# Kernel tuning notes

Measured on AMD Instinct MI355X. Metric: run time of the kernel, lower is better.

The kernel has to match this reference:

```python
import jax, jax.numpy as jnp
import numpy as np

BETA = 0.25  # commitment_beta


def setup_inputs() -> dict:
    key = jax.random.key(0)
    k1, k2 = jax.random.split(key)
    x = jax.random.normal(k1, (16, 256, 32, 32), dtype=jnp.float32)
    # codebook weight: (n_embed + 1, embed_dim); last row is the padding idx (zeros)
    weight = jax.random.normal(k2, (8193, 256), dtype=jnp.float32) * 0.05
    weight = weight.at[-1].set(0.0)
    return {"x": x, "weight": weight}


def reference(x, weight):
    # Eval-mode forward of VectorQuantize2 (accept_image_fmap=True, no EMA update).
    B, C, H, W = x.shape
    xf = jnp.transpose(x, (0, 2, 3, 1)).reshape(B, H * W, C)  # b (h w) c
    emb = weight[:-1]  # [N, C], drop padding row
    # squared euclidean distance; argmin identical to torch.cdist argmin
    d2 = (
        jnp.sum(xf * xf, axis=-1, keepdims=True)
        - 2.0 * jnp.einsum("bnc,kc->bnk", xf, emb)
        + jnp.sum(emb * emb, axis=-1)
    )  # [B, HW, N]
    code = jnp.argmin(d2, axis=-1)  # [B, HW]
    x_q = emb[code]  # [B, HW, C]
    loss = BETA * jnp.mean((jax.lax.stop_gradient(x_q) - xf) ** 2) + jnp.mean(
        (x_q - jax.lax.stop_gradient(xf)) ** 2
    )
    # straight-through estimator
    xq_st = xf + jax.lax.stop_gradient(x_q - xf)
    xq_out = jnp.transpose(xq_st.reshape(B, H, W, C), (0, 3, 1, 2))  # b c h w
    code_out = code.reshape(B, H, W)
    return xq_out, loss, code_out
```

## Files before the change

### kernel.cpp

```cpp
#include <hip/hip_runtime.h>
#include <hip/hip_bf16.h>


#define N_ROWS   16384
#define KCODES   8192
#define DIM      256
#define LOSS_OFF 4194304
#define CODE_OFF 4194305
#define MARGIN_ACC 0.006f

typedef _Float16 half8  __attribute__((ext_vector_type(8)));
typedef _Float16 half4v __attribute__((ext_vector_type(4)));
typedef float    float4v __attribute__((ext_vector_type(4)));
typedef unsigned long long u64;

__device__ __forceinline__ unsigned umax32(unsigned a, unsigned b) { return a > b ? a : b; }
__device__ __forceinline__ unsigned umin32(unsigned a, unsigned b) { return a < b ? a : b; }
__device__ __forceinline__ void gll16(const _Float16* g, _Float16* l) {
  __builtin_amdgcn_global_load_lds((const __attribute__((address_space(1))) void*)g,
                                   (__attribute__((address_space(3))) void*)l, 16, 0, 0);
}


__global__ __launch_bounds__(256) void k_prep(const float* __restrict__ x, _Float16* __restrict__ xh,
                                              const float* __restrict__ wt, _Float16* __restrict__ eh,
                                              float* __restrict__ en2c, float* __restrict__ sxxp,
                                              double* __restrict__ dacc, unsigned* __restrict__ cnt) {
  __shared__ float lsx[128 * 65];
  __shared__ __align__(16) _Float16 ls[8192];
  __shared__ float es[32];
  int t = threadIdx.x;
  int lane = t & 63, wv = t >> 6;
  int bid = blockIdx.x;
  if (bid < 512) {
    if (bid == 0 && t == 0) { dacc[0] = 0.0; *cnt = 0u; }
    int blk = bid >> 2, cc = bid & 3;
    int row0 = blk * 128;
    int b    = row0 >> 10;
    int n0   = row0 & 1023;
    const float* xb = x + (size_t)b * 262144 + n0;
    int n_l = t & 127, cg = t >> 7;
    float sxx = 0.f;
    for (int j = 0; j < 32; ++j) {
      int c = cc * 64 + cg * 32 + j;
      float v = xb[(size_t)c * 1024 + n_l];
      sxx = fmaf(v, v, sxx);
      lsx[n_l * 65 + (c & 63)] = v;
    }
    __syncthreads();
#pragma unroll
    for (int i = 0; i < 4; ++i) {
      int unit = i * 256 + t;
      int rl = unit >> 3, p = unit & 7;
      const float* src = &lsx[rl * 65 + p * 8];
      half8 h;
#pragma unroll
      for (int k2 = 0; k2 < 8; ++k2) h[k2] = (_Float16)src[k2];
      int p7 = p ^ (rl & 7);
      *(half8*)&xh[(size_t)blk * 32768 + (size_t)cc * 8192 + (size_t)rl * 64 + p7 * 8] = h;
    }
#pragma unroll
    for (int d = 32; d; d >>= 1) sxx += __shfl_xor(sxx, d);
    __syncthreads();
    if (lane == 0) lsx[wv] = sxx;
    __syncthreads();
    if (t == 0) sxxp[bid] = lsx[0] + lsx[1] + lsx[2] + lsx[3];
  } else {
    int blk  = bid - 512;
    int k0 = blk * 32;
    const float* wb = wt + (size_t)k0 * 256;
    for (int i = 0; i < 8; ++i) {
      int lin = i * 1024 + t * 4;
      float4v v = *(const float4v*)&wb[lin];
      half4v h; float ss = 0.f;
#pragma unroll
      for (int j = 0; j < 4; ++j) { h[j] = (_Float16)v[j]; ss = fmaf(v[j], v[j], ss); }
      *(half4v*)&ls[lin] = h;
#pragma unroll
      for (int d = 32; d; d >>= 1) ss += __shfl_xor(ss, d);
      if (lane == 0) es[i * 4 + wv] = ss;
    }
    __syncthreads();
    size_t tb = (size_t)(k0 >> 7) * 32768;
    for (int i = 0; i < 4; ++i) {
      int u = i * 256 + t;
      int code_l = u >> 5;
      int cu = u & 31, chunk = cu >> 3, p = cu & 7;
      int kgl = k0 + code_l;
      int kg = p ^ (kgl & 7);
      half8 h = *(half8*)&ls[code_l * 256 + chunk * 64 + kg * 8];
      *(half8*)&eh[tb + (size_t)chunk * 8192 + (size_t)(kgl & 127) * 64 + p * 8] = h;
    }
    if (t < 32) en2c[k0 + t] = 32.0f - 0.5f * es[t];
  }
}

__global__ __launch_bounds__(256) void k_gemm(const _Float16* __restrict__ xh, const _Float16* __restrict__ eh,
                                              const float* __restrict__ en2c,
                                              u64* __restrict__ top2) {
  __shared__ __align__(16) _Float16 As[8192];
  __shared__ __align__(16) _Float16 Bs[8192];
  int t    = threadIdx.x;
  int bx   = blockIdx.x;
  int by   = blockIdx.y;
  int lane = t & 63, w = t >> 6;
  int wr = w & 1, wc = w >> 1;
  int ln15 = lane & 15, q = lane >> 4;
  int q4 = q * 4;

  const _Float16* Ag = eh + (size_t)bx * 32768;
  const _Float16* Bg = xh + (size_t)by * 32768;

  int kwave = bx * 128 + wr * 64;
  float4v cin[4];
#pragma unroll
  for (int mi = 0; mi < 4; ++mi) cin[mi] = *(const float4v*)&en2c[kwave + mi * 16 + q4];

  float4v acc[4][4];
#pragma unroll
  for (int mi = 0; mi < 4; ++mi)
#pragma unroll
    for (int ni = 0; ni < 4; ++ni) acc[mi][ni] = cin[mi];

  int so = (w * 64 + lane) * 8;
  int lo = w * 512;

  for (int ch = 0; ch < 4; ++ch) {
    if (ch) __syncthreads();
    const _Float16* ac = Ag + ch * 8192;
    const _Float16* bc = Bg + ch * 8192;
#pragma unroll
    for (int i = 0; i < 4; ++i) {
      gll16(ac + i * 2048 + so, As + i * 2048 + lo);
      gll16(bc + i * 2048 + so, Bs + i * 2048 + lo);
    }
    __syncthreads();
#pragma unroll
    for (int ks = 0; ks < 2; ++ks) {
      half8 af[4], bf[4];
#pragma unroll
      for (int mi = 0; mi < 4; ++mi) {
        int row = wr * 64 + mi * 16 + ln15;
        af[mi] = *(const half8*)&As[(row * 8 + ((ks * 4 + q) ^ (row & 7))) * 8];
      }
#pragma unroll
      for (int ni = 0; ni < 4; ++ni) {
        int row = wc * 64 + ni * 16 + ln15;
        bf[ni] = *(const half8*)&Bs[(row * 8 + ((ks * 4 + q) ^ (row & 7))) * 8];
      }
#pragma unroll
      for (int mi = 0; mi < 4; ++mi)
#pragma unroll
        for (int ni = 0; ni < 4; ++ni)
          acc[mi][ni] = __builtin_amdgcn_mfma_f32_16x16x32_f16(af[mi], bf[ni], acc[mi][ni], 0, 0, 0);
    }
  }

  __syncthreads();
  u64* ep = (u64*)(void*)As;
  int ibase = wr * 64 + q4;

#pragma unroll
  for (int ni = 0; ni < 4; ++ni) {
    unsigned hi[8], lo2[8];
#pragma unroll
    for (int j = 0; j < 8; ++j) {
      int mi = j >> 1, rb = (j & 1) * 2;
      unsigned p0 = (__float_as_uint(acc[mi][ni][rb])     & 0xFFFFFF80u) | (unsigned)(ibase + mi * 16 + rb);
      unsigned p1 = (__float_as_uint(acc[mi][ni][rb + 1]) & 0xFFFFFF80u) | (unsigned)(ibase + mi * 16 + rb + 1);
      hi[j] = umax32(p0, p1); lo2[j] = umin32(p0, p1);
    }
#pragma unroll
    for (int st = 4; st; st >>= 1)
#pragma unroll
      for (int j = 0; j < 8; ++j) if (j < st) {
        unsigned nb = umax32(hi[j], hi[j + st]);
        unsigned ns = umax32(umin32(hi[j], hi[j + st]), umax32(lo2[j], lo2[j + st]));
        hi[j] = nb; lo2[j] = ns;
      }
    unsigned b = hi[0], s = lo2[0];
#pragma unroll
    for (int d = 16; d < 64; d <<= 1) {
      unsigned ob = __shfl_xor(b, d);
      unsigned os = __shfl_xor(s, d);
      unsigned ns = umax32(umin32(b, ob), umax32(s, os));
      b = umax32(b, ob); s = ns;
    }
    if (q == 0) {
      int rl = wc * 64 + ni * 16 + ln15;
      ep[rl * 2 + wr] = ((u64)b << 32) | s;
    }
  }
  __syncthreads();
  if (t < 128) {
    u64 A = ep[t * 2 + 0], B = ep[t * 2 + 1];
    unsigned a0 = (unsigned)(A >> 32), a1 = (unsigned)A;
    unsigned b0 = (unsigned)(B >> 32), b1 = (unsigned)B;
    unsigned best = umax32(a0, b0);
    unsigned sec  = umax32(umin32(a0, b0), umax32(a1, b1));
    top2[(size_t)bx * 16384 + (size_t)by * 128 + t] = ((u64)best << 32) | sec;
  }
}

__global__ __launch_bounds__(1024) void k_out(const u64* __restrict__ top2,
                                              const float* __restrict__ x, const float* __restrict__ w,
                                              float* __restrict__ out, const float* __restrict__ sxxp,
                                              double* __restrict__ dacc, unsigned* __restrict__ cnt) {
  __shared__ float ect[256 * 65];
  __shared__ double dpart[16];
  __shared__ unsigned oldc;
  int t    = threadIdx.x;
  int lane = t & 63, wv = t >> 6;
  int blk  = blockIdx.x;
  int row0 = blk * 64;
  int b = row0 >> 10, n0 = row0 & 1023;

  double dsum = 0.0;
  for (int j = 0; j < 4; ++j) {
    int rl  = wv * 4 + j;
    int row = row0 + rl;
    u64 e = top2[(size_t)lane * 16384 + row];
    unsigned hi = (unsigned)(e >> 32), lo = (unsigned)e;
    unsigned mx = hi;
#pragma unroll
    for (int d = 1; d < 64; d <<= 1) mx = umax32(mx, __shfl_xor(mx, d));
    float fm = __uint_as_float(mx & 0xFFFFFF80u);
    float th = fm - MARGIN_ACC;
    bool c0 = __uint_as_float(hi & 0xFFFFFF80u) >= th;
    bool c1 = __uint_as_float(lo & 0xFFFFFF80u) >= th;
    u64 bal0 = __ballot(c0), bal1 = __ballot(c1);
    int kbest;
    double d2c;
    if (__popcll(bal0) + __popcll(bal1) <= 1) {
      int l0 = __ffsll((unsigned long long)__ballot(hi == mx)) - 1;
      kbest = l0 * 128 + (int)(__shfl(hi, l0) & 127u);
      d2c = 64.0 - 2.0 * (double)fm;
    } else {
      const float* xr = x + (size_t)b * 262144 + (row & 1023);
      float4v ex;
#pragma unroll
      for (int i = 0; i < 4; ++i) ex[i] = xr[(size_t)(lane * 4 + i) * 1024];
      double bs = 1e300; int bk = 0x7fffffff;
      for (int pass = 0; pass < 2; ++pass) {
        u64 bal = pass ? bal1 : bal0;
        unsigned src = pass ? lo : hi;
        while (bal) {
          int l = __ffsll((unsigned long long)bal) - 1;
          bal &= bal - 1;
          int kc = l * 128 + (int)(__shfl(src, l) & 127u);
          float4v wv4 = *(const float4v*)&w[(size_t)kc * DIM + lane * 4];
          double s = 0.0;
#pragma unroll
          for (int i = 0; i < 4; ++i) { double ev = (double)wv4[i]; s += ev * (ev - 2.0 * (double)ex[i]); }
#pragma unroll
          for (int d = 1; d < 64; d <<= 1) s += __shfl_xor(s, d);
          if (s < bs || (s == bs && kc < bk)) { bs = s; bk = kc; }
        }
      }
      kbest = bk;
      d2c = bs;
    }
    if (lane == 0) { out[CODE_OFF + row] = (float)kbest; dsum += d2c; }
    const float* wrow = w + (size_t)kbest * 256;
#pragma unroll
    for (int i = 0; i < 4; ++i) ect[(i * 64 + lane) * 65 + rl] = wrow[i * 64 + lane];
  }
  __syncthreads();

  const size_t base = (size_t)b * 262144 + n0 + lane;
  for (int j = 0; j < 16; ++j) {
    int c = wv * 16 + j;
    out[base + (size_t)c * 1024] = ect[c * 65 + lane];
  }
  if (lane == 0) dpart[wv] = dsum;
  __syncthreads();
  if (t == 0) {
    double s = 0.0;
#pragma unroll
    for (int i = 0; i < 16; ++i) s += dpart[i];
    atomicAdd(&dacc[0], s);
    __threadfence();
    oldc = atomicAdd(cnt, 1u);
  }
  __syncthreads();
  if (oldc == 255u && t < 64) {
    float ps = 0.f;
#pragma unroll
    for (int i = 0; i < 8; ++i) ps += sxxp[t * 8 + i];
#pragma unroll
    for (int d = 32; d; d >>= 1) ps += __shfl_xor(ps, d);
    if (t == 0) {
      __threadfence();
      double sd2 = *(volatile double*)&dacc[0];
      out[LOSS_OFF] = (float)(1.25 * ((double)ps + sd2) / 4194304.0);
    }
  }
}

extern "C" void kernel_launch(void* const* d_in, const int* in_sizes, int n_in,
                              void* d_out, int out_size, void* d_ws, size_t ws_size,
                              hipStream_t stream) {
  const float* x = (const float*)d_in[0];
  const float* w = (const float*)d_in[1];
  float* out = (float*)d_out;
  char* ws = (char*)d_ws;
  _Float16* xh   = (_Float16*)(ws);
  _Float16* eh   = (_Float16*)(ws + 8388608);
  float*    en2c = (float*)(ws + 12582912);
  u64*      top2 = (u64*)(ws + 12615680);
  float*    sxxp = (float*)(ws + 21004288);
  double*   dacc = (double*)(ws + 21006336);
  unsigned* cnt  = (unsigned*)(ws + 21006344);

  k_prep<<<768, 256, 0, stream>>>(x, xh, w, eh, en2c, sxxp, dacc, cnt);
  k_gemm<<<dim3(64, 128), 256, 0, stream>>>(xh, eh, en2c, top2);
  k_out<<<256, 1024, 0, stream>>>(top2, x, w, out, sxxp, dacc, cnt);
}
```

Before: 172.6 us.

## Enlarge GEMM tiles to 256x256 with double-buffered LDS prefetch and block swizzle

Rewrites the distance GEMM so each 512-thread block computes a 256x256 tile with 8 waves, double-buffering LDS so the next K chunk loads while MFMAs run. It adds wave priority boosting around MFMA bursts, a block-index swizzle for L2 locality, and writes per-wave top-2 partials straight to global memory instead of merging through LDS. The aim is to raise arithmetic intensity and hide global-load latency. The cost is much larger LDS and register use per block, which may limit occupancy.

```diff
diff --git a/kernel.cpp b/kernel.cpp
--- a/kernel.cpp
+++ b/kernel.cpp
@@ -19,6 +19,11 @@
 __device__ __forceinline__ void gll16(const _Float16* g, _Float16* l) {
   __builtin_amdgcn_global_load_lds((const __attribute__((address_space(1))) void*)g,
                                    (__attribute__((address_space(3))) void*)l, 16, 0, 0);
+}
+
+__device__ __forceinline__ void stage16k(const _Float16* __restrict__ g, _Float16* l, int t, int w) {
+  gll16(g + t * 8,        l + w * 512);
+  gll16(g + 4096 + t * 8, l + 4096 + w * 512);
 }
 
 
@@ -95,83 +100,105 @@
   }
 }
 
-__global__ __launch_bounds__(256) void k_gemm(const _Float16* __restrict__ xh, const _Float16* __restrict__ eh,
-                                              const float* __restrict__ en2c,
-                                              u64* __restrict__ top2) {
-  __shared__ __align__(16) _Float16 As[8192];
-  __shared__ __align__(16) _Float16 Bs[8192];
+__global__ __launch_bounds__(512, 2) void k_gemm(const _Float16* __restrict__ xh, const _Float16* __restrict__ eh,
+                                                 const float* __restrict__ en2c,
+                                                 u64* __restrict__ top2) {
+  __shared__ __align__(16) _Float16 As[2][16384];
+  __shared__ __align__(16) _Float16 Bs[2][16384];
   int t    = threadIdx.x;
-  int bx   = blockIdx.x;
-  int by   = blockIdx.y;
   int lane = t & 63, w = t >> 6;
-  int wr = w & 1, wc = w >> 1;
-  int ln15 = lane & 15, q = lane >> 4;
+  int wr = w >> 2, wc = w & 3;
+  int ln15 = lane & 15, q = (lane >> 4) & 3;
   int q4 = q * 4;
 
-  const _Float16* Ag = eh + (size_t)bx * 32768;
-  const _Float16* Bg = xh + (size_t)by * 32768;
-
-  int kwave = bx * 128 + wr * 64;
-  float4v cin[4];
-#pragma unroll
-  for (int mi = 0; mi < 4; ++mi) cin[mi] = *(const float4v*)&en2c[kwave + mi * 16 + q4];
-
-  float4v acc[4][4];
-#pragma unroll
-  for (int mi = 0; mi < 4; ++mi)
-#pragma unroll
-    for (int ni = 0; ni < 4; ++ni) acc[mi][ni] = cin[mi];
-
-  int so = (w * 64 + lane) * 8;
-  int lo = w * 512;
-
-  for (int ch = 0; ch < 4; ++ch) {
-    if (ch) __syncthreads();
-    const _Float16* ac = Ag + ch * 8192;
-    const _Float16* bc = Bg + ch * 8192;
-#pragma unroll
-    for (int i = 0; i < 4; ++i) {
-      gll16(ac + i * 2048 + so, As + i * 2048 + lo);
-      gll16(bc + i * 2048 + so, Bs + i * 2048 + lo);
-    }
-    __syncthreads();
-#pragma unroll
-    for (int ks = 0; ks < 2; ++ks) {
-      half8 af[4], bf[4];
-#pragma unroll
-      for (int mi = 0; mi < 4; ++mi) {
-        int row = wr * 64 + mi * 16 + ln15;
-        af[mi] = *(const half8*)&As[(row * 8 + ((ks * 4 + q) ^ (row & 7))) * 8];
-      }
-#pragma unroll
-      for (int ni = 0; ni < 4; ++ni) {
-        int row = wc * 64 + ni * 16 + ln15;
-        bf[ni] = *(const half8*)&Bs[(row * 8 + ((ks * 4 + q) ^ (row & 7))) * 8];
-      }
-#pragma unroll
-      for (int mi = 0; mi < 4; ++mi)
+  int orig = (int)blockIdx.y * 32 + (int)blockIdx.x;
+  int swz  = (orig & 7) * 256 + (orig >> 3);
+  int bx = swz & 31;
+  int by = swz >> 5;
+
+  const _Float16* Ag0 = eh + (size_t)(2 * bx)     * 32768;
+  const _Float16* Ag1 = eh + (size_t)(2 * bx + 1) * 32768;
+  const _Float16* Bg0 = xh + (size_t)(2 * by)     * 32768;
+  const _Float16* Bg1 = xh + (size_t)(2 * by + 1) * 32768;
+
+  float4v acc[8][4];
+#pragma unroll
+  for (int mi = 0; mi < 8; ++mi) {
+    float4v cin = *(const float4v*)&en2c[bx * 256 + wr * 128 + mi * 16 + q4];
+#pragma unroll
+    for (int ni = 0; ni < 4; ++ni) acc[mi][ni] = cin;
+  }
+
+  stage16k(Ag0, &As[0][0],    t, w);
+  stage16k(Ag1, &As[0][8192], t, w);
+  stage16k(Bg0, &Bs[0][0],    t, w);
+  stage16k(Bg1, &Bs[0][8192], t, w);
+  asm volatile("s_waitcnt vmcnt(0)" ::: "memory");
+  __builtin_amdgcn_s_barrier();
+
+#pragma unroll
+  for (int kt = 0; kt < 4; ++kt) {
+    const int d = kt & 1;
+    const _Float16* Ac = &As[d][0];
+    const _Float16* Bc = &Bs[d][0];
+    _Float16* An = &As[d ^ 1][0];
+    _Float16* Bn = &Bs[d ^ 1][0];
+    half8 bf[4];
+#pragma unroll
+    for (int p = 0; p < 4; ++p) {
+      const int ks = p >> 1, mih = p & 1;
+      half8 af[4];
+#pragma unroll
+      for (int m2 = 0; m2 < 4; ++m2) {
+        int rl = (mih * 4 + m2) * 16 + ln15;
+        af[m2] = *(const half8*)&Ac[wr * 8192 + rl * 64 + (((ks * 4 + q) ^ (rl & 7)) * 8)];
+      }
+      if (mih == 0) {
+#pragma unroll
+        for (int ni = 0; ni < 4; ++ni) {
+          int rb = (wc & 1) * 64 + ni * 16 + ln15;
+          bf[ni] = *(const half8*)&Bc[(wc >> 1) * 8192 + rb * 64 + (((ks * 4 + q) ^ (rb & 7)) * 8)];
+        }
+      }
+      if (kt < 3) {
+        if (p == 0) stage16k(Ag0 + (kt + 1) * 8192, An,        t, w);
+        if (p == 1) stage16k(Ag1 + (kt + 1) * 8192, An + 8192, t, w);
+        if (p == 2) stage16k(Bg0 + (kt + 1) * 8192, Bn,        t, w);
+        if (p == 3) stage16k(Bg1 + (kt + 1) * 8192, Bn + 8192, t, w);
+      }
+      __builtin_amdgcn_s_barrier();
+      asm volatile("s_waitcnt lgkmcnt(0)");
+      __builtin_amdgcn_s_setprio(1);
+#pragma unroll
+      for (int m2 = 0; m2 < 4; ++m2)
 #pragma unroll
         for (int ni = 0; ni < 4; ++ni)
-          acc[mi][ni] = __builtin_amdgcn_mfma_f32_16x16x32_f16(af[mi], bf[ni], acc[mi][ni], 0, 0, 0);
-    }
-  }
-
-  __syncthreads();
-  u64* ep = (u64*)(void*)As;
-  int ibase = wr * 64 + q4;
+          acc[mih * 4 + m2][ni] =
+              __builtin_amdgcn_mfma_f32_16x16x32_f16(af[m2], bf[ni], acc[mih * 4 + m2][ni], 0, 0, 0);
+      __builtin_amdgcn_s_setprio(0);
+      __builtin_amdgcn_s_barrier();
+    }
+    if (kt < 3) {
+      asm volatile("s_waitcnt vmcnt(0)" ::: "memory");
+      __builtin_amdgcn_sched_barrier(0);
+      __builtin_amdgcn_s_barrier();
+    }
+  }
 
 #pragma unroll
   for (int ni = 0; ni < 4; ++ni) {
-    unsigned hi[8], lo2[8];
-#pragma unroll
-    for (int j = 0; j < 8; ++j) {
-      int mi = j >> 1, rb = (j & 1) * 2;
-      unsigned p0 = (__float_as_uint(acc[mi][ni][rb])     & 0xFFFFFF80u) | (unsigned)(ibase + mi * 16 + rb);
-      unsigned p1 = (__float_as_uint(acc[mi][ni][rb + 1]) & 0xFFFFFF80u) | (unsigned)(ibase + mi * 16 + rb + 1);
-      hi[j] = umax32(p0, p1); lo2[j] = umin32(p0, p1);
-    }
-#pragma unroll
-    for (int st = 4; st; st >>= 1)
+    unsigned hi[16], lo2[16];
+#pragma unroll
+    for (int mi = 0; mi < 8; ++mi)
+#pragma unroll
+      for (int rb = 0; rb < 4; rb += 2) {
+        int j = mi * 2 + (rb >> 1);
+        unsigned p0 = (__float_as_uint(acc[mi][ni][rb])     & 0xFFFFFF80u) | (unsigned)(mi * 16 + q4 + rb);
+        unsigned p1 = (__float_as_uint(acc[mi][ni][rb + 1]) & 0xFFFFFF80u) | (unsigned)(mi * 16 + q4 + rb + 1);
+        hi[j] = umax32(p0, p1); lo2[j] = umin32(p0, p1);
+      }
+#pragma unroll
+    for (int st = 8; st; st >>= 1)
 #pragma unroll
       for (int j = 0; j < 8; ++j) if (j < st) {
         unsigned nb = umax32(hi[j], hi[j + st]);
@@ -180,25 +207,16 @@
       }
     unsigned b = hi[0], s = lo2[0];
 #pragma unroll
-    for (int d = 16; d < 64; d <<= 1) {
-      unsigned ob = __shfl_xor(b, d);
-      unsigned os = __shfl_xor(s, d);
+    for (int dd = 16; dd < 64; dd <<= 1) {
+      unsigned ob = __shfl_xor(b, dd);
+      unsigned os = __shfl_xor(s, dd);
       unsigned ns = umax32(umin32(b, ob), umax32(s, os));
       b = umax32(b, ob); s = ns;
     }
     if (q == 0) {
-      int rl = wc * 64 + ni * 16 + ln15;
-      ep[rl * 2 + wr] = ((u64)b << 32) | s;
-    }
-  }
-  __syncthreads();
-  if (t < 128) {
-    u64 A = ep[t * 2 + 0], B = ep[t * 2 + 1];
-    unsigned a0 = (unsigned)(A >> 32), a1 = (unsigned)A;
-    unsigned b0 = (unsigned)(B >> 32), b1 = (unsigned)B;
-    unsigned best = umax32(a0, b0);
-    unsigned sec  = umax32(umin32(a0, b0), umax32(a1, b1));
-    top2[(size_t)bx * 16384 + (size_t)by * 128 + t] = ((u64)best << 32) | sec;
+      int row = by * 256 + wc * 64 + ni * 16 + ln15;
+      top2[(size_t)(bx * 2 + wr) * 16384 + row] = ((u64)b << 32) | s;
+    }
   }
 }
 
@@ -313,6 +331,6 @@
   unsigned* cnt  = (unsigned*)(ws + 21006344);
 
   k_prep<<<768, 256, 0, stream>>>(x, xh, w, eh, en2c, sxxp, dacc, cnt);
-  k_gemm<<<dim3(64, 128), 256, 0, stream>>>(xh, eh, en2c, top2);
+  k_gemm<<<dim3(32, 64), 512, 0, stream>>>(xh, eh, en2c, top2);
   k_out<<<256, 1024, 0, stream>>>(top2, x, w, out, sxxp, dacc, cnt);
 }
```

Result: slower. 186.2 us (+7.9%).
